# Optimization experiments

Hardware: AMD Instinct MI355X
Metric: run time of the kernel (lower is better)

The kernel has to match this reference:

```python
import jax, jax.numpy as jnp
import numpy as np

N_CAT = 100000
N_USERS = 50000
N_REL = 32
D = 64
E = 1600000
NNZ = 1000000


def setup_inputs() -> dict:
    key = jax.random.key(0)
    ks = jax.random.split(key, 8)
    category_emb = jax.random.normal(ks[0], (N_CAT, D), dtype=jnp.float32)
    user_emb = jax.random.normal(ks[1], (N_USERS, D), dtype=jnp.float32)
    edge_index = jax.random.randint(ks[2], (2, E), 0, N_CAT, dtype=jnp.int64)
    edge_type = jax.random.randint(ks[3], (E,), 1, N_REL + 1, dtype=jnp.int64)  # 1-indexed relations
    im_rows = jax.random.randint(ks[4], (NNZ,), 0, N_USERS, dtype=jnp.int64)
    im_cols = jax.random.randint(ks[5], (NNZ,), 0, N_CAT, dtype=jnp.int64)
    im_vals = jax.random.uniform(ks[6], (NNZ,), dtype=jnp.float32)
    weight = jax.random.normal(ks[7], (N_REL, D), dtype=jnp.float32)
    return {"category_emb": category_emb, "user_emb": user_emb,
            "edge_index": edge_index, "edge_type": edge_type,
            "im_rows": im_rows, "im_cols": im_cols, "im_vals": im_vals,
            "weight": weight}


def reference(category_emb, user_emb, edge_index, edge_type, im_rows, im_cols, im_vals, weight):
    n_categories = category_emb.shape[0]
    n_users = user_emb.shape[0]
    head, tail = edge_index[0], edge_index[1]

    edge_relation_emb = weight[edge_type - 1]                      # [E, D]
    neigh_relation_emb = category_emb[tail] * edge_relation_emb    # [E, D]

    # attention weight: (||h*r|| * ||t*r||)^2 per edge -> scalar per edge
    hr = jnp.linalg.norm(category_emb[head] * edge_relation_emb, axis=1)  # [E]
    tr = jnp.linalg.norm(neigh_relation_emb, axis=1)                      # [E]
    att = (hr * tr) ** 2                                                  # [E]

    # scatter_softmax over edges grouped by head node
    grp_max = jax.ops.segment_max(att, head, num_segments=n_categories)   # [N_CAT]
    e = jnp.exp(att - grp_max[head])                                      # [E]
    grp_sum = jax.ops.segment_sum(e, head, num_segments=n_categories)     # [N_CAT]
    w = e / grp_sum[head]                                                 # [E]

    # scatter_sum aggregation to heads
    category_agg = jax.ops.segment_sum(w[:, None] * neigh_relation_emb,
                                       head, num_segments=n_categories)   # [N_CAT, D]

    # sparse interact_mat @ category_emb (COO)
    user_agg = jax.ops.segment_sum(im_vals[:, None] * category_emb[im_cols],
                                   im_rows, num_segments=n_users)         # [N_USERS, D]

    score = jax.nn.softmax(user_emb @ weight.T, axis=-1)                   # [N_USERS, N_REL]
    user_agg = user_agg + (score @ weight) * user_agg
    return (category_agg, user_agg)
```

## Files before the change

### kernel.cpp

```cpp
#include <hip/hip_runtime.h>
#include <hip/hip_bf16.h>
#include <hip/hip_fp16.h>
#include <float.h>
#include <stdint.h>

#define N_CAT   100000
#define N_USERS 50000
#define N_REL   32
#define D       64
#define NEDGE   1600000
#define NNZ     1000000

#define EB_SHIFT 9
#define EB_SIZE  512
#define NBKE     ((N_CAT + EB_SIZE - 1) / EB_SIZE)
#define UB_SHIFT 8
#define UB_SIZE  256
#define NBKU     ((N_USERS + UB_SIZE - 1) / UB_SIZE)
#define NBK      (NBKE + NBKU)

#define T1   4096
#define ECAP 15360
#define UCAP 7680

#define WSTRIDE 17


__device__ __forceinline__ unsigned int pack_half2(float a, float b) {
    return (unsigned int)__half_as_ushort(__float2half_rn(a)) |
           ((unsigned int)__half_as_ushort(__float2half_rn(b)) << 16);
}

template<int F16>
__device__ __forceinline__ void load_row8(const float4* __restrict__ catv4,
                                          const uint4* __restrict__ cath4,
                                          int row, int gl, float f[8]) {
    if (F16) {
        uint4 h = cath4[(size_t)row * 8 + gl];
        const __half2* hp = (const __half2*)&h;
        float2 a = __half22float2(hp[0]);
        float2 b = __half22float2(hp[1]);
        float2 c = __half22float2(hp[2]);
        float2 d = __half22float2(hp[3]);
        f[0] = a.x; f[1] = a.y; f[2] = b.x; f[3] = b.y;
        f[4] = c.x; f[5] = c.y; f[6] = d.x; f[7] = d.y;
    } else {
        float4 a = catv4[(size_t)row * 16 + gl * 2];
        float4 b = catv4[(size_t)row * 16 + gl * 2 + 1];
        f[0] = a.x; f[1] = a.y; f[2] = a.z; f[3] = a.w;
        f[4] = b.x; f[5] = b.y; f[6] = b.z; f[7] = b.w;
    }
}

__device__ __forceinline__ float reduce_scatter8(const float a[8], int lane) {
    int b3 = (lane >> 3) & 1, b4 = (lane >> 4) & 1, b5 = (lane >> 5) & 1;
    float r[4];
#pragma unroll
    for (int j = 0; j < 4; ++j) {
        float x = b3 ? a[j] : a[j + 4];
        float k = b3 ? a[j + 4] : a[j];
        r[j] = k + __shfl_xor(x, 8);
    }
    float s[2];
#pragma unroll
    for (int j = 0; j < 2; ++j) {
        float x = b4 ? r[j] : r[j + 2];
        float k = b4 ? r[j + 2] : r[j];
        s[j] = k + __shfl_xor(x, 16);
    }
    float x = b5 ? s[0] : s[1];
    float k = b5 ? s[1] : s[0];
    return k + __shfl_xor(x, 32);
}

__device__ __forceinline__ int dim_of_lane(int lane) {
    int g = lane >> 3;
    return ((lane & 7) << 3) | ((g & 1) << 2) | (g & 2) | (g >> 2);
}

template<int W16>
__global__ __launch_bounds__(256) void norm2_kernel(
        const float* __restrict__ cat,
        const float* __restrict__ W,
        float* __restrict__ norm2,
        unsigned short* __restrict__ cath) {
    __shared__ float4 w2[N_REL * 16];
    int t = threadIdx.x;
    const float4* Wv = (const float4*)W;
    for (int i = t; i < N_REL * 16; i += 256) {
        float4 v = Wv[i];
        v.x *= v.x; v.y *= v.y; v.z *= v.z; v.w *= v.w;
        w2[i] = v;
    }
    __syncthreads();

    int node = blockIdx.x * 64 + (t >> 2);
    int q    = t & 3;
    if (node >= N_CAT) return;

    const float4* catv = (const float4*)cat;
    float acc[N_REL];
#pragma unroll
    for (int r = 0; r < N_REL; ++r) acc[r] = 0.f;

    uint2 hp[4];
#pragma unroll
    for (int c = 0; c < 4; ++c) {
        float4 xv = catv[(size_t)node * 16 + q * 4 + c];
        if (W16) {
            hp[c].x = pack_half2(xv.x, xv.y);
            hp[c].y = pack_half2(xv.z, xv.w);
        }
        xv.x *= xv.x; xv.y *= xv.y; xv.z *= xv.z; xv.w *= xv.w;
#pragma unroll
        for (int r = 0; r < N_REL; ++r) {
            float4 wv = w2[r * 16 + q * 4 + c];
            acc[r] += xv.x * wv.x + xv.y * wv.y + xv.z * wv.z + xv.w * wv.w;
        }
    }
    if (W16) {
        uint4* cv16 = (uint4*)cath;
        cv16[(size_t)node * 8 + q * 2]     = make_uint4(hp[0].x, hp[0].y, hp[1].x, hp[1].y);
        cv16[(size_t)node * 8 + q * 2 + 1] = make_uint4(hp[2].x, hp[2].y, hp[3].x, hp[3].y);
    }
#pragma unroll
    for (int r = 0; r < N_REL; ++r) {
        acc[r] += __shfl_xor(acc[r], 1);
        acc[r] += __shfl_xor(acc[r], 2);
    }
    float4* nv = (float4*)norm2;
    size_t base = (size_t)node * 8 + q * 2;
    if (q == 0) {
        nv[base]     = make_float4(acc[0],  acc[1],  acc[2],  acc[3]);
        nv[base + 1] = make_float4(acc[4],  acc[5],  acc[6],  acc[7]);
    } else if (q == 1) {
        nv[base]     = make_float4(acc[8],  acc[9],  acc[10], acc[11]);
        nv[base + 1] = make_float4(acc[12], acc[13], acc[14], acc[15]);
    } else if (q == 2) {
        nv[base]     = make_float4(acc[16], acc[17], acc[18], acc[19]);
        nv[base + 1] = make_float4(acc[20], acc[21], acc[22], acc[23]);
    } else {
        nv[base]     = make_float4(acc[24], acc[25], acc[26], acc[27]);
        nv[base + 1] = make_float4(acc[28], acc[29], acc[30], acc[31]);
    }
}

__global__ void coarse_hist_kernel(const int* __restrict__ head,
                                   const int* __restrict__ imr,
                                   int* __restrict__ ccnt) {
    __shared__ int h[NBK];
    int t = threadIdx.x;
    for (int i = t; i < NBK; i += 256) h[i] = 0;
    __syncthreads();
    int stride = gridDim.x * 256;
    for (int i = blockIdx.x * 256 + t; i < NEDGE + NNZ; i += stride) {
        if (i < NEDGE) atomicAdd(&h[head[i] >> EB_SHIFT], 1);
        else           atomicAdd(&h[NBKE + (imr[i - NEDGE] >> UB_SHIFT)], 1);
    }
    __syncthreads();
    for (int i = t; i < NBK; i += 256) if (h[i]) atomicAdd(&ccnt[i], h[i]);
}

__global__ void coarse_scan_kernel(const int* __restrict__ ccnt,
                                   int* __restrict__ cbase_e, int* __restrict__ cbase_u,
                                   int* __restrict__ ccur_e,  int* __restrict__ ccur_u,
                                   int* __restrict__ offs_e,  int* __restrict__ offs_u) {
    __shared__ int sc[256];
    int t = threadIdx.x;
    int c = (t < NBKE) ? ccnt[t] : 0;
    sc[t] = c; __syncthreads();
    for (int off = 1; off < 256; off <<= 1) {
        int v = (t >= off) ? sc[t - off] : 0; __syncthreads();
        sc[t] += v; __syncthreads();
    }
    int excl = sc[t] - c;
    if (t < NBKE) { cbase_e[t] = excl; ccur_e[t] = excl; }
    if (t == NBKE - 1) cbase_e[NBKE] = excl + c;
    __syncthreads();
    c = (t < NBKU) ? ccnt[NBKE + t] : 0;
    sc[t] = c; __syncthreads();
    for (int off = 1; off < 256; off <<= 1) {
        int v = (t >= off) ? sc[t - off] : 0; __syncthreads();
        sc[t] += v; __syncthreads();
    }
    excl = sc[t] - c;
    if (t < NBKU) { cbase_u[t] = excl; ccur_u[t] = excl; }
    if (t == NBKU - 1) cbase_u[NBKU] = excl + c;
    if (t == 0) { offs_e[N_CAT] = NEDGE; offs_u[N_USERS] = NNZ; }
}

__global__ __launch_bounds__(256) void pass1_edges_kernel(
        const int* __restrict__ head, const int* __restrict__ tail,
        const int* __restrict__ etype, int* __restrict__ ccur_e,
        int* __restrict__ sorted_ta) {
    __shared__ int cnt[256], loc[256], base[256], sc[256];
    __shared__ int stage[T1];
    __shared__ int gpos[T1];
    int t = threadIdx.x;
    int tile = blockIdx.x * T1;
    cnt[t] = 0;
    __syncthreads();
    int rec[16], bk[16];
#pragma unroll
    for (int k = 0; k < 16; ++k) {
        int i = tile + k * 256 + t;
        if (i < NEDGE) {
            int h = head[i], tl = tail[i], r = etype[i] - 1;
            bk[k]  = h >> EB_SHIFT;
            rec[k] = ((h & (EB_SIZE - 1)) << 22) | (tl << 5) | r;
            atomicAdd(&cnt[bk[k]], 1);
        } else bk[k] = -1;
    }
    __syncthreads();
    int c = cnt[t];
    sc[t] = c; __syncthreads();
    for (int off = 1; off < 256; off <<= 1) {
        int v = (t >= off) ? sc[t - off] : 0; __syncthreads();
        sc[t] += v; __syncthreads();
    }
    loc[t] = sc[t] - c;
    if (t < NBKE && c > 0) base[t] = atomicAdd(&ccur_e[t], c);
    __syncthreads();
    cnt[t] = loc[t];
    __syncthreads();
#pragma unroll
    for (int k = 0; k < 16; ++k) {
        if (bk[k] >= 0) {
            int p = atomicAdd(&cnt[bk[k]], 1);
            stage[p] = rec[k];
            gpos[p]  = base[bk[k]] + (p - loc[bk[k]]);
        }
    }
    __syncthreads();
    int nv = min(T1, NEDGE - tile);
    for (int i = t; i < nv; i += 256) sorted_ta[gpos[i]] = stage[i];
}

__global__ __launch_bounds__(256) void pass1_users_kernel(
        const int* __restrict__ imr, const int* __restrict__ imc,
        const float* __restrict__ imv, int* __restrict__ ccur_u,
        int2* __restrict__ sorted_cv) {
    __shared__ int cnt[256], loc[256], base[256], sc[256];
    __shared__ int2 stage[T1];
    __shared__ int gpos[T1];
    int t = threadIdx.x;
    int tile = blockIdx.x * T1;
    cnt[t] = 0;
    __syncthreads();
    int2 rec[16]; int bk[16];
#pragma unroll
    for (int k = 0; k < 16; ++k) {
        int i = tile + k * 256 + t;
        if (i < NNZ) {
            int rr = imr[i];
            bk[k]  = rr >> UB_SHIFT;
            rec[k] = make_int2(((rr & (UB_SIZE - 1)) << 17) | imc[i],
                               __float_as_int(imv[i]));
            atomicAdd(&cnt[bk[k]], 1);
        } else bk[k] = -1;
    }
    __syncthreads();
    int c = cnt[t];
    sc[t] = c; __syncthreads();
    for (int off = 1; off < 256; off <<= 1) {
        int v = (t >= off) ? sc[t - off] : 0; __syncthreads();
        sc[t] += v; __syncthreads();
    }
    loc[t] = sc[t] - c;
    if (t < NBKU && c > 0) base[t] = atomicAdd(&ccur_u[t], c);
    __syncthreads();
    cnt[t] = loc[t];
    __syncthreads();
#pragma unroll
    for (int k = 0; k < 16; ++k) {
        if (bk[k] >= 0) {
            int p = atomicAdd(&cnt[bk[k]], 1);
            stage[p] = rec[k];
            gpos[p]  = base[bk[k]] + (p - loc[bk[k]]);
        }
    }
    __syncthreads();
    int nv = min(T1, NNZ - tile);
    for (int i = t; i < nv; i += 256) sorted_cv[gpos[i]] = stage[i];
}

__global__ __launch_bounds__(256) void pass2_kernel(
        const int* __restrict__ cbase_e, const int* __restrict__ cbase_u,
        int* __restrict__ offs_e, int* __restrict__ offs_u,
        int* __restrict__ sorted_ta, int2* __restrict__ sorted_cv) {
    __shared__ int lds[UCAP * 2];
    __shared__ int fh[EB_SIZE + 1];
    __shared__ int sc[256];
    int t = threadIdx.x;
    int b = blockIdx.x;
    if (b < NBKE) {
        int h0 = b << EB_SHIFT;
        int start = cbase_e[b], end = cbase_e[b + 1];
        int n = min(end - start, ECAP);
        for (int i = t; i < n; i += 256) lds[i] = sorted_ta[start + i];
        fh[2 * t] = 0; fh[2 * t + 1] = 0;
        __syncthreads();
        for (int i = t; i < n; i += 256) atomicAdd(&fh[lds[i] >> 22], 1);
        __syncthreads();
        int a = fh[2 * t], b2 = fh[2 * t + 1];
        sc[t] = a + b2; __syncthreads();
        for (int off = 1; off < 256; off <<= 1) {
            int v = (t >= off) ? sc[t - off] : 0; __syncthreads();
            sc[t] += v; __syncthreads();
        }
        int pe = sc[t] - (a + b2);
        int lim = min(EB_SIZE, N_CAT - h0);
        if (2 * t     < lim) offs_e[h0 + 2 * t]     = start + pe;
        if (2 * t + 1 < lim) offs_e[h0 + 2 * t + 1] = start + pe + a;
        fh[2 * t] = pe; fh[2 * t + 1] = pe + a;
        __syncthreads();
        for (int i = t; i < n; i += 256) {
            int rec = lds[i];
            int p = atomicAdd(&fh[rec >> 22], 1);
            sorted_ta[start + p] = rec & 0x3FFFFF;
        }
    } else {
        int k = b - NBKE;
        int u0 = k << UB_SHIFT;
        int start = cbase_u[k], end = cbase_u[k + 1];
        int n = min(end - start, UCAP);
        int2* lds2 = (int2*)lds;
        for (int i = t; i < n; i += 256) lds2[i] = sorted_cv[start + i];
        fh[t] = 0;
        __syncthreads();
        for (int i = t; i < n; i += 256) atomicAdd(&fh[lds2[i].x >> 17], 1);
        __syncthreads();
        int c = fh[t];
        sc[t] = c; __syncthreads();
        for (int off = 1; off < 256; off <<= 1) {
            int v = (t >= off) ? sc[t - off] : 0; __syncthreads();
            sc[t] += v; __syncthreads();
        }
        int excl = sc[t] - c;
        int lim = min(UB_SIZE, N_USERS - u0);
        if (t < lim) offs_u[u0 + t] = start + excl;
        fh[t] = excl;
        __syncthreads();
        for (int i = t; i < n; i += 256) {
            int2 rec = lds2[i];
            int p = atomicAdd(&fh[rec.x >> 17], 1);
            sorted_cv[start + p] = make_int2(rec.x & 0x1FFFF, rec.y);
        }
    }
}

#define FMA8(ACC, WS, F, W0, W1)                                         \
    ACC[0] += WS * F[0] * W0.x;  ACC[1] += WS * F[1] * W0.y;             \
    ACC[2] += WS * F[2] * W0.z;  ACC[3] += WS * F[3] * W0.w;             \
    ACC[4] += WS * F[4] * W1.x;  ACC[5] += WS * F[5] * W1.y;             \
    ACC[6] += WS * F[6] * W1.z;  ACC[7] += WS * F[7] * W1.w;

__global__ __launch_bounds__(256) void scale_kernel(
        const float* __restrict__ uemb,
        const float* __restrict__ W,
        float* __restrict__ uagg) {
    __shared__ float4 sW[N_REL * 16];
    int t = threadIdx.x;
    const float4* Wv = (const float4*)W;
    for (int i = t; i < N_REL * 16; i += 256) sW[i] = Wv[i];
    __syncthreads();

    int u = blockIdx.x * 64 + (t >> 2);
    int q = t & 3;
    if (u >= N_USERS) return;

    const float4* ur4 = (const float4*)(uemb + (size_t)u * D);
    float acc[N_REL];
#pragma unroll
    for (int r = 0; r < N_REL; ++r) acc[r] = 0.f;

#pragma unroll 1
    for (int c = 0; c < 4; ++c) {
        float4 uv = ur4[q * 4 + c];
#pragma unroll 4
        for (int r = 0; r < N_REL; ++r) {
            float4 w4 = sW[r * 16 + q * 4 + c];
            acc[r] += uv.x * w4.x + uv.y * w4.y + uv.z * w4.z + uv.w * w4.w;
        }
    }
#pragma unroll
    for (int r = 0; r < N_REL; ++r) {
        acc[r] += __shfl_xor(acc[r], 1);
        acc[r] += __shfl_xor(acc[r], 2);
    }
    float m = acc[0];
#pragma unroll
    for (int r = 1; r < N_REL; ++r) m = fmaxf(m, acc[r]);
    float s = 0.f;
#pragma unroll
    for (int r = 0; r < N_REL; ++r) { acc[r] = __expf(acc[r] - m); s += acc[r]; }
    float inv = 1.f / s;

    float4* out4 = (float4*)(uagg + (size_t)u * D);
#pragma unroll 1
    for (int c = 0; c < 4; ++c) {
        float px = 0.f, py = 0.f, pz = 0.f, pw = 0.f;
#pragma unroll 4
        for (int r = 0; r < N_REL; ++r) {
            float4 w4 = sW[r * 16 + c * 4 + q];
            px += acc[r] * w4.x; py += acc[r] * w4.y;
            pz += acc[r] * w4.z; pw += acc[r] * w4.w;
        }
        out4[c * 4 + q] = make_float4(1.f + px * inv, 1.f + py * inv,
                                      1.f + pz * inv, 1.f + pw * inv);
    }
}

template<int F16>
__global__ __launch_bounds__(256, 4) void cat_agg_sorted_kernel(
        const int* __restrict__ offs_e,
        const int* __restrict__ sorted_ta,
        const float* __restrict__ norm2,
        const float* __restrict__ cat,
        const uint4* __restrict__ cath4,
        const float* __restrict__ W,
        float* __restrict__ cat_agg) {
    __shared__ float4 sW4[N_REL * WSTRIDE];
    __shared__ float  scr[4][D];
    {
        const float4* Wv = (const float4*)W;
        for (int i = threadIdx.x; i < N_REL * 16; i += 256)
            sW4[(i >> 4) * WSTRIDE + (i & 15)] = Wv[i];
    }
    __syncthreads();

    const float4* catv4 = (const float4*)cat;
    int wv   = threadIdx.x >> 6;
    int lane = threadIdx.x & 63;
    int grp  = lane >> 3;
    int gl   = lane & 7;
    int h = blockIdx.x * 4 + wv;
    int start = offs_e[h];
    int end   = offs_e[h + 1];
    int deg   = end - start;

    float accA[8], accB[8];
#pragma unroll
    for (int k = 0; k < 8; ++k) { accA[k] = 0.f; accB[k] = 0.f; }

    if (deg <= 32) {
        int rec = 0;
        if (lane < deg) rec = sorted_ta[start + lane];
        int tt = rec >> 5, r = rec & 31;
        float n2t = norm2[(size_t)tt * N_REL + r];
        float n2h = norm2[(size_t)h  * N_REL + r];

        int tA0 = __shfl(rec, grp),      tB0 = __shfl(rec, 8 + grp);
        float fA0[8], fB0[8], fA1[8], fB1[8];
        load_row8<F16>(catv4, cath4, tA0 >> 5, gl, fA0);
        load_row8<F16>(catv4, cath4, tB0 >> 5, gl, fB0);
        int tA1 = 0, tB1 = 0;
        if (deg > 16) {
            tA1 = __shfl(rec, 16 + grp); tB1 = __shfl(rec, 24 + grp);
            load_row8<F16>(catv4, cath4, tA1 >> 5, gl, fA1);
            load_row8<F16>(catv4, cath4, tB1 >> 5, gl, fB1);
        }

        float att = (lane < deg) ? n2h * n2t : -FLT_MAX;
        float m = att;
        m = fmaxf(m, __shfl_xor(m, 1));
        m = fmaxf(m, __shfl_xor(m, 2));
        m = fmaxf(m, __shfl_xor(m, 4));
        m = fmaxf(m, __shfl_xor(m, 8));
        if (deg > 16) m = fmaxf(m, __shfl_xor(m, 16));
        float ex = (lane < deg) ? __expf(att - m) : 0.f;
        float ssum = ex;
        ssum += __shfl_xor(ssum, 1);
        ssum += __shfl_xor(ssum, 2);
        ssum += __shfl_xor(ssum, 4);
        ssum += __shfl_xor(ssum, 8);
        if (deg > 16) ssum += __shfl_xor(ssum, 16);
        float w = (deg > 0) ? ex / ssum : 0.f;

        float wA0 = __shfl(w, grp), wB0 = __shfl(w, 8 + grp);
        const float4* wrA0 = &sW4[(tA0 & 31) * WSTRIDE + gl * 2];
        const float4* wrB0 = &sW4[(tB0 & 31) * WSTRIDE + gl * 2];
        float4 wa00 = wrA0[0], wa01 = wrA0[1];
        float4 wb00 = wrB0[0], wb01 = wrB0[1];
        FMA8(accA, wA0, fA0, wa00, wa01)
        FMA8(accB, wB0, fB0, wb00, wb01)
        if (deg > 16) {
            float wA1 = __shfl(w, 16 + grp), wB1 = __shfl(w, 24 + grp);
            const float4* wrA1 = &sW4[(tA1 & 31) * WSTRIDE + gl * 2];
            const float4* wrB1 = &sW4[(tB1 & 31) * WSTRIDE + gl * 2];
            float4 wa10 = wrA1[0], wa11 = wrA1[1];
            float4 wb10 = wrB1[0], wb11 = wrB1[1];
            FMA8(accA, wA1, fA1, wa10, wa11)
            FMA8(accB, wB1, fB1, wb10, wb11)
        }
    } else if (deg <= 64) {
        int   rec = 0;
        float att = -FLT_MAX;
        if (lane < deg) {
            rec = sorted_ta[start + lane];
            int tt = rec >> 5, r = rec & 31;
            att = norm2[h * N_REL + r] * norm2[(size_t)tt * N_REL + r];
        }
        float m = att;
#pragma unroll
        for (int off = 32; off > 0; off >>= 1) m = fmaxf(m, __shfl_xor(m, off));
        float ex = (lane < deg) ? __expf(att - m) : 0.f;
        float ssum = ex;
#pragma unroll
        for (int off = 32; off > 0; off >>= 1) ssum += __shfl_xor(ssum, off);
        float w = (deg > 0) ? ex / ssum : 0.f;

        for (int e = 0; e < deg; e += 16) {
            int   tA = __shfl(rec, e + grp);
            float wA = __shfl(w,   e + grp);
            int   tB = __shfl(rec, e + 8 + grp);
            float wB = __shfl(w,   e + 8 + grp);
            float fA[8], fB[8];
            load_row8<F16>(catv4, cath4, tA >> 5, gl, fA);
            load_row8<F16>(catv4, cath4, tB >> 5, gl, fB);
            const float4* wrA = &sW4[(tA & 31) * WSTRIDE + gl * 2];
            const float4* wrB = &sW4[(tB & 31) * WSTRIDE + gl * 2];
            float4 wa0 = wrA[0], wa1 = wrA[1];
            float4 wb0 = wrB[0], wb1 = wrB[1];
            FMA8(accA, wA, fA, wa0, wa1)
            FMA8(accB, wB, fB, wb0, wb1)
        }
    } else {
        float m = -FLT_MAX;
        for (int j = lane; j < deg; j += 64) {
            int rec = sorted_ta[start + j];
            int tt = rec >> 5, r = rec & 31;
            m = fmaxf(m, norm2[h * N_REL + r] * norm2[(size_t)tt * N_REL + r]);
        }
#pragma unroll
        for (int off = 32; off > 0; off >>= 1) m = fmaxf(m, __shfl_xor(m, off));
        float ssum = 0.f;
        for (int j = lane; j < deg; j += 64) {
            int rec = sorted_ta[start + j];
            int tt = rec >> 5, r = rec & 31;
            ssum += __expf(norm2[h * N_REL + r] * norm2[(size_t)tt * N_REL + r] - m);
        }
#pragma unroll
        for (int off = 32; off > 0; off >>= 1) ssum += __shfl_xor(ssum, off);
        float inv = 1.f / ssum;
        for (int j0 = 0; j0 < deg; j0 += 64) {
            int n = min(64, deg - j0);
            int   rec = 0;
            float w   = 0.f;
            if (lane < n) {
                rec = sorted_ta[start + j0 + lane];
                int tt = rec >> 5, r = rec & 31;
                w = __expf(norm2[h * N_REL + r] * norm2[(size_t)tt * N_REL + r] - m) * inv;
            }
            for (int e = 0; e < n; e += 16) {
                int   tA = __shfl(rec, e + grp);
                float wA = __shfl(w,   e + grp);
                int   tB = __shfl(rec, e + 8 + grp);
                float wB = __shfl(w,   e + 8 + grp);
                float fA[8], fB[8];
                load_row8<F16>(catv4, cath4, tA >> 5, gl, fA);
                load_row8<F16>(catv4, cath4, tB >> 5, gl, fB);
                const float4* wrA = &sW4[(tA & 31) * WSTRIDE + gl * 2];
                const float4* wrB = &sW4[(tB & 31) * WSTRIDE + gl * 2];
                float4 wa0 = wrA[0], wa1 = wrA[1];
                float4 wb0 = wrB[0], wb1 = wrB[1];
                FMA8(accA, wA, fA, wa0, wa1)
                FMA8(accB, wB, fB, wb0, wb1)
            }
        }
    }

    float a[8];
#pragma unroll
    for (int k = 0; k < 8; ++k) a[k] = accA[k] + accB[k];
    float tot = reduce_scatter8(a, lane);
    scr[wv][dim_of_lane(lane)] = tot;
    if (lane < 16) {
        float4 o = ((const float4*)scr[wv])[lane];
        ((float4*)&cat_agg[(size_t)h * D])[lane] = o;
    }
}

template<int F16>
__global__ __launch_bounds__(256, 4) void spmm_user_kernel(
        const int* __restrict__ offs_u,
        const int2* __restrict__ sorted_cv,
        const float* __restrict__ cat,
        const uint4* __restrict__ cath4,
        float* __restrict__ uagg) {
    __shared__ float scr[4][D];
    const float4* catv4 = (const float4*)cat;
    int wv   = threadIdx.x >> 6;
    int lane = threadIdx.x & 63;
    int grp  = lane >> 3;
    int gl   = lane & 7;
    int u = blockIdx.x * 4 + wv;
    int start = offs_u[u];
    int end   = offs_u[u + 1];
    int deg   = end - start;

    float accA[8], accB[8];
#pragma unroll
    for (int k = 0; k < 8; ++k) { accA[k] = 0.f; accB[k] = 0.f; }

    if (deg <= 32) {
        int my_c = 0; float my_v = 0.f;
        if (lane < deg) {
            int2 cv = sorted_cv[start + lane];
            my_c = cv.x;
            my_v = __int_as_float(cv.y);
        }
        int   cA0 = __shfl(my_c, grp),     cB0 = __shfl(my_c, 8 + grp);
        float vA0 = __shfl(my_v, grp),     vB0 = __shfl(my_v, 8 + grp);
        float fA0[8], fB0[8], fA1[8], fB1[8];
        load_row8<F16>(catv4, cath4, cA0, gl, fA0);
        load_row8<F16>(catv4, cath4, cB0, gl, fB0);
        float vA1 = 0.f, vB1 = 0.f;
        if (deg > 16) {
            int cA1 = __shfl(my_c, 16 + grp), cB1 = __shfl(my_c, 24 + grp);
            vA1 = __shfl(my_v, 16 + grp); vB1 = __shfl(my_v, 24 + grp);
            load_row8<F16>(catv4, cath4, cA1, gl, fA1);
            load_row8<F16>(catv4, cath4, cB1, gl, fB1);
#pragma unroll
            for (int k = 0; k < 8; ++k) {
                accA[k] += vA1 * fA1[k];
                accB[k] += vB1 * fB1[k];
            }
        }
#pragma unroll
        for (int k = 0; k < 8; ++k) {
            accA[k] += vA0 * fA0[k];
            accB[k] += vB0 * fB0[k];
        }
    } else {
        for (int j0 = 0; j0 < deg; j0 += 64) {
            int n = min(64, deg - j0);
            int   my_c = 0;
            float my_v = 0.f;
            if (lane < n) {
                int2 cv = sorted_cv[start + j0 + lane];
                my_c = cv.x;
                my_v = __int_as_float(cv.y);
            }
            for (int e = 0; e < n; e += 16) {
                int   cA = __shfl(my_c, e + grp);
                float vA = __shfl(my_v, e + grp);
                int   cB = __shfl(my_c, e + 8 + grp);
                float vB = __shfl(my_v, e + 8 + grp);
                float fA[8], fB[8];
                load_row8<F16>(catv4, cath4, cA, gl, fA);
                load_row8<F16>(catv4, cath4, cB, gl, fB);
#pragma unroll
                for (int k = 0; k < 8; ++k) {
                    accA[k] += vA * fA[k];
                    accB[k] += vB * fB[k];
                }
            }
        }
    }

    float a[8];
#pragma unroll
    for (int k = 0; k < 8; ++k) a[k] = accA[k] + accB[k];
    float tot = reduce_scatter8(a, lane);
    scr[wv][dim_of_lane(lane)] = tot;
    if (lane < 16) {
        float4 o = ((const float4*)scr[wv])[lane];
        float4* row = (float4*)&uagg[(size_t)u * D];
        float4 s = row[lane];
        row[lane] = make_float4(o.x * s.x, o.y * s.y, o.z * s.z, o.w * s.w);
    }
}

extern "C" void kernel_launch(void* const* d_in, const int* in_sizes, int n_in,
                              void* d_out, int out_size, void* d_ws, size_t ws_size,
                              hipStream_t stream) {
    const float* cat   = (const float*)d_in[0];
    const float* uemb  = (const float*)d_in[1];
    const int*   eidx  = (const int*)d_in[2];
    const int*   etype = (const int*)d_in[3];
    const int*   imr   = (const int*)d_in[4];
    const int*   imc   = (const int*)d_in[5];
    const float* imv   = (const float*)d_in[6];
    const float* W     = (const float*)d_in[7];
    const int* head = eidx;
    const int* tail = eidx + NEDGE;

    float* out     = (float*)d_out;
    float* cat_agg = out;
    float* uagg    = out + (size_t)N_CAT * D;

    float* norm2   = (float*)d_ws;
    int*   ccnt    = (int*)(norm2 + (size_t)N_CAT * N_REL);
    int*   cbase_e = ccnt + NBK;
    int*   cbase_u = cbase_e + NBKE + 1;
    int*   ccur_e  = cbase_u + NBKU + 1;
    int*   ccur_u  = ccur_e + NBKE;
    int*   offs_e  = ccur_u + NBKU;
    int*   offs_u  = offs_e + N_CAT + 1;
    int*   sorted_ta = offs_u + N_USERS + 1;
    int2*  sorted_cv = (int2*)(sorted_ta + NEDGE);

    unsigned short* cath_us =
        (unsigned short*)(((uintptr_t)(sorted_cv + NNZ) + 255) & ~(uintptr_t)255);
    size_t need = (size_t)((char*)(cath_us + (size_t)N_CAT * D) - (char*)d_ws);
    int use16 = (ws_size >= need);

    hipMemsetAsync(ccnt, 0, (size_t)NBK * sizeof(int), stream);

    coarse_hist_kernel<<<512, 256, 0, stream>>>(head, imr, ccnt);
    coarse_scan_kernel<<<1, 256, 0, stream>>>(ccnt, cbase_e, cbase_u,
                                              ccur_e, ccur_u, offs_e, offs_u);
    pass1_edges_kernel<<<(NEDGE + T1 - 1) / T1, 256, 0, stream>>>(
        head, tail, etype, ccur_e, sorted_ta);
    pass1_users_kernel<<<(NNZ + T1 - 1) / T1, 256, 0, stream>>>(
        imr, imc, imv, ccur_u, sorted_cv);
    pass2_kernel<<<NBK, 256, 0, stream>>>(cbase_e, cbase_u, offs_e, offs_u,
                                          sorted_ta, sorted_cv);
    scale_kernel<<<(N_USERS + 63) / 64, 256, 0, stream>>>(uemb, W, uagg);
    if (use16) {
        norm2_kernel<1><<<(N_CAT + 63) / 64, 256, 0, stream>>>(cat, W, norm2, cath_us);
        cat_agg_sorted_kernel<1><<<N_CAT / 4, 256, 0, stream>>>(
            offs_e, sorted_ta, norm2, cat, (const uint4*)cath_us, W, cat_agg);
        spmm_user_kernel<1><<<N_USERS / 4, 256, 0, stream>>>(
            offs_u, sorted_cv, cat, (const uint4*)cath_us, uagg);
    } else {
        norm2_kernel<0><<<(N_CAT + 63) / 64, 256, 0, stream>>>(cat, W, norm2, nullptr);
        cat_agg_sorted_kernel<0><<<N_CAT / 4, 256, 0, stream>>>(
            offs_e, sorted_ta, norm2, cat, nullptr, W, cat_agg);
        spmm_user_kernel<0><<<N_USERS / 4, 256, 0, stream>>>(
            offs_u, sorted_cv, cat, nullptr, uagg);
    }
}
```

Baseline: 310.2 us.

## Replace two-level bucket sort with global-atomic counting sort for CSR build

Replaces the coarse-bucket histogram, LDS-staged pass1 scatter and per-bucket pass2 refinement with a fine-grained global-atomic histogram, a two-block scan of per-node counts, and a direct atomic scatter into final CSR positions. This cuts kernel launches and the second read/write pass over the sorted arrays. In exchange it issues heavily contended global atomics, runs a serial-chunk scan in only two blocks, and makes uncoalesced random writes. Edge order within a segment also becomes nondeterministic, which can change float summation order.

```diff
diff --git a/kernel.cpp b/kernel.cpp
--- a/kernel.cpp
+++ b/kernel.cpp
@@ -10,18 +10,6 @@
 #define D       64
 #define NEDGE   1600000
 #define NNZ     1000000
-
-#define EB_SHIFT 9
-#define EB_SIZE  512
-#define NBKE     ((N_CAT + EB_SIZE - 1) / EB_SIZE)
-#define UB_SHIFT 8
-#define UB_SIZE  256
-#define NBKU     ((N_USERS + UB_SIZE - 1) / UB_SIZE)
-#define NBK      (NBKE + NBKU)
-
-#define T1   4096
-#define ECAP 15360
-#define UCAP 7680
 
 #define WSTRIDE 17
 
@@ -145,206 +133,64 @@
     }
 }
 
-__global__ void coarse_hist_kernel(const int* __restrict__ head,
-                                   const int* __restrict__ imr,
-                                   int* __restrict__ ccnt) {
-    __shared__ int h[NBK];
+__global__ __launch_bounds__(256) void hist_kernel(
+        const int* __restrict__ head, const int* __restrict__ imr,
+        int* __restrict__ cnt_e, int* __restrict__ cnt_u) {
+    int stride = gridDim.x * 256;
+    for (int i = blockIdx.x * 256 + threadIdx.x; i < NEDGE + NNZ; i += stride) {
+        if (i < NEDGE) atomicAdd(&cnt_e[head[i]], 1);
+        else           atomicAdd(&cnt_u[imr[i - NEDGE]], 1);
+    }
+}
+
+__device__ __forceinline__ void scan_one(const int* __restrict__ cnt, int n,
+                                         int* __restrict__ offs,
+                                         int* __restrict__ cur) {
+    __shared__ int part[1024];
     int t = threadIdx.x;
-    for (int i = t; i < NBK; i += 256) h[i] = 0;
-    __syncthreads();
+    int chunk = (n + 1023) / 1024;
+    int lo = t * chunk, hi = min(lo + chunk, n);
+    int s = 0;
+    for (int i = lo; i < hi; ++i) s += cnt[i];
+    part[t] = s; __syncthreads();
+    for (int off = 1; off < 1024; off <<= 1) {
+        int v = (t >= off) ? part[t - off] : 0; __syncthreads();
+        part[t] += v; __syncthreads();
+    }
+    int base = part[t] - s;
+    for (int i = lo; i < hi; ++i) {
+        offs[i] = base; cur[i] = base;
+        base += cnt[i];
+    }
+    if (t == 1023) offs[n] = part[1023];
+}
+
+__global__ __launch_bounds__(1024) void scan2_kernel(
+        const int* __restrict__ cnt_e, const int* __restrict__ cnt_u,
+        int* __restrict__ offs_e, int* __restrict__ offs_u,
+        int* __restrict__ cur_e,  int* __restrict__ cur_u) {
+    if (blockIdx.x == 0) scan_one(cnt_e, N_CAT,   offs_e, cur_e);
+    else                 scan_one(cnt_u, N_USERS, offs_u, cur_u);
+}
+
+__global__ __launch_bounds__(256) void scatter_kernel(
+        const int* __restrict__ head, const int* __restrict__ tail,
+        const int* __restrict__ etype,
+        const int* __restrict__ imr, const int* __restrict__ imc,
+        const float* __restrict__ imv,
+        int* __restrict__ cur_e, int* __restrict__ cur_u,
+        int* __restrict__ sorted_ta, int2* __restrict__ sorted_cv) {
     int stride = gridDim.x * 256;
-    for (int i = blockIdx.x * 256 + t; i < NEDGE + NNZ; i += stride) {
-        if (i < NEDGE) atomicAdd(&h[head[i] >> EB_SHIFT], 1);
-        else           atomicAdd(&h[NBKE + (imr[i - NEDGE] >> UB_SHIFT)], 1);
-    }
-    __syncthreads();
-    for (int i = t; i < NBK; i += 256) if (h[i]) atomicAdd(&ccnt[i], h[i]);
-}
-
-__global__ void coarse_scan_kernel(const int* __restrict__ ccnt,
-                                   int* __restrict__ cbase_e, int* __restrict__ cbase_u,
-                                   int* __restrict__ ccur_e,  int* __restrict__ ccur_u,
-                                   int* __restrict__ offs_e,  int* __restrict__ offs_u) {
-    __shared__ int sc[256];
-    int t = threadIdx.x;
-    int c = (t < NBKE) ? ccnt[t] : 0;
-    sc[t] = c; __syncthreads();
-    for (int off = 1; off < 256; off <<= 1) {
-        int v = (t >= off) ? sc[t - off] : 0; __syncthreads();
-        sc[t] += v; __syncthreads();
-    }
-    int excl = sc[t] - c;
-    if (t < NBKE) { cbase_e[t] = excl; ccur_e[t] = excl; }
-    if (t == NBKE - 1) cbase_e[NBKE] = excl + c;
-    __syncthreads();
-    c = (t < NBKU) ? ccnt[NBKE + t] : 0;
-    sc[t] = c; __syncthreads();
-    for (int off = 1; off < 256; off <<= 1) {
-        int v = (t >= off) ? sc[t - off] : 0; __syncthreads();
-        sc[t] += v; __syncthreads();
-    }
-    excl = sc[t] - c;
-    if (t < NBKU) { cbase_u[t] = excl; ccur_u[t] = excl; }
-    if (t == NBKU - 1) cbase_u[NBKU] = excl + c;
-    if (t == 0) { offs_e[N_CAT] = NEDGE; offs_u[N_USERS] = NNZ; }
-}
-
-__global__ __launch_bounds__(256) void pass1_edges_kernel(
-        const int* __restrict__ head, const int* __restrict__ tail,
-        const int* __restrict__ etype, int* __restrict__ ccur_e,
-        int* __restrict__ sorted_ta) {
-    __shared__ int cnt[256], loc[256], base[256], sc[256];
-    __shared__ int stage[T1];
-    __shared__ int gpos[T1];
-    int t = threadIdx.x;
-    int tile = blockIdx.x * T1;
-    cnt[t] = 0;
-    __syncthreads();
-    int rec[16], bk[16];
-#pragma unroll
-    for (int k = 0; k < 16; ++k) {
-        int i = tile + k * 256 + t;
+    for (int i = blockIdx.x * 256 + threadIdx.x; i < NEDGE + NNZ; i += stride) {
         if (i < NEDGE) {
-            int h = head[i], tl = tail[i], r = etype[i] - 1;
-            bk[k]  = h >> EB_SHIFT;
-            rec[k] = ((h & (EB_SIZE - 1)) << 22) | (tl << 5) | r;
-            atomicAdd(&cnt[bk[k]], 1);
-        } else bk[k] = -1;
-    }
-    __syncthreads();
-    int c = cnt[t];
-    sc[t] = c; __syncthreads();
-    for (int off = 1; off < 256; off <<= 1) {
-        int v = (t >= off) ? sc[t - off] : 0; __syncthreads();
-        sc[t] += v; __syncthreads();
-    }
-    loc[t] = sc[t] - c;
-    if (t < NBKE && c > 0) base[t] = atomicAdd(&ccur_e[t], c);
-    __syncthreads();
-    cnt[t] = loc[t];
-    __syncthreads();
-#pragma unroll
-    for (int k = 0; k < 16; ++k) {
-        if (bk[k] >= 0) {
-            int p = atomicAdd(&cnt[bk[k]], 1);
-            stage[p] = rec[k];
-            gpos[p]  = base[bk[k]] + (p - loc[bk[k]]);
-        }
-    }
-    __syncthreads();
-    int nv = min(T1, NEDGE - tile);
-    for (int i = t; i < nv; i += 256) sorted_ta[gpos[i]] = stage[i];
-}
-
-__global__ __launch_bounds__(256) void pass1_users_kernel(
-        const int* __restrict__ imr, const int* __restrict__ imc,
-        const float* __restrict__ imv, int* __restrict__ ccur_u,
-        int2* __restrict__ sorted_cv) {
-    __shared__ int cnt[256], loc[256], base[256], sc[256];
-    __shared__ int2 stage[T1];
-    __shared__ int gpos[T1];
-    int t = threadIdx.x;
-    int tile = blockIdx.x * T1;
-    cnt[t] = 0;
-    __syncthreads();
-    int2 rec[16]; int bk[16];
-#pragma unroll
-    for (int k = 0; k < 16; ++k) {
-        int i = tile + k * 256 + t;
-        if (i < NNZ) {
-            int rr = imr[i];
-            bk[k]  = rr >> UB_SHIFT;
-            rec[k] = make_int2(((rr & (UB_SIZE - 1)) << 17) | imc[i],
-                               __float_as_int(imv[i]));
-            atomicAdd(&cnt[bk[k]], 1);
-        } else bk[k] = -1;
-    }
-    __syncthreads();
-    int c = cnt[t];
-    sc[t] = c; __syncthreads();
-    for (int off = 1; off < 256; off <<= 1) {
-        int v = (t >= off) ? sc[t - off] : 0; __syncthreads();
-        sc[t] += v; __syncthreads();
-    }
-    loc[t] = sc[t] - c;
-    if (t < NBKU && c > 0) base[t] = atomicAdd(&ccur_u[t], c);
-    __syncthreads();
-    cnt[t] = loc[t];
-    __syncthreads();
-#pragma unroll
-    for (int k = 0; k < 16; ++k) {
-        if (bk[k] >= 0) {
-            int p = atomicAdd(&cnt[bk[k]], 1);
-            stage[p] = rec[k];
-            gpos[p]  = base[bk[k]] + (p - loc[bk[k]]);
-        }
-    }
-    __syncthreads();
-    int nv = min(T1, NNZ - tile);
-    for (int i = t; i < nv; i += 256) sorted_cv[gpos[i]] = stage[i];
-}
-
-__global__ __launch_bounds__(256) void pass2_kernel(
-        const int* __restrict__ cbase_e, const int* __restrict__ cbase_u,
-        int* __restrict__ offs_e, int* __restrict__ offs_u,
-        int* __restrict__ sorted_ta, int2* __restrict__ sorted_cv) {
-    __shared__ int lds[UCAP * 2];
-    __shared__ int fh[EB_SIZE + 1];
-    __shared__ int sc[256];
-    int t = threadIdx.x;
-    int b = blockIdx.x;
-    if (b < NBKE) {
-        int h0 = b << EB_SHIFT;
-        int start = cbase_e[b], end = cbase_e[b + 1];
-        int n = min(end - start, ECAP);
-        for (int i = t; i < n; i += 256) lds[i] = sorted_ta[start + i];
-        fh[2 * t] = 0; fh[2 * t + 1] = 0;
-        __syncthreads();
-        for (int i = t; i < n; i += 256) atomicAdd(&fh[lds[i] >> 22], 1);
-        __syncthreads();
-        int a = fh[2 * t], b2 = fh[2 * t + 1];
-        sc[t] = a + b2; __syncthreads();
-        for (int off = 1; off < 256; off <<= 1) {
-            int v = (t >= off) ? sc[t - off] : 0; __syncthreads();
-            sc[t] += v; __syncthreads();
-        }
-        int pe = sc[t] - (a + b2);
-        int lim = min(EB_SIZE, N_CAT - h0);
-        if (2 * t     < lim) offs_e[h0 + 2 * t]     = start + pe;
-        if (2 * t + 1 < lim) offs_e[h0 + 2 * t + 1] = start + pe + a;
-        fh[2 * t] = pe; fh[2 * t + 1] = pe + a;
-        __syncthreads();
-        for (int i = t; i < n; i += 256) {
-            int rec = lds[i];
-            int p = atomicAdd(&fh[rec >> 22], 1);
-            sorted_ta[start + p] = rec & 0x3FFFFF;
-        }
-    } else {
-        int k = b - NBKE;
-        int u0 = k << UB_SHIFT;
-        int start = cbase_u[k], end = cbase_u[k + 1];
-        int n = min(end - start, UCAP);
-        int2* lds2 = (int2*)lds;
-        for (int i = t; i < n; i += 256) lds2[i] = sorted_cv[start + i];
-        fh[t] = 0;
-        __syncthreads();
-        for (int i = t; i < n; i += 256) atomicAdd(&fh[lds2[i].x >> 17], 1);
-        __syncthreads();
-        int c = fh[t];
-        sc[t] = c; __syncthreads();
-        for (int off = 1; off < 256; off <<= 1) {
-            int v = (t >= off) ? sc[t - off] : 0; __syncthreads();
-            sc[t] += v; __syncthreads();
-        }
-        int excl = sc[t] - c;
-        int lim = min(UB_SIZE, N_USERS - u0);
-        if (t < lim) offs_u[u0 + t] = start + excl;
-        fh[t] = excl;
-        __syncthreads();
-        for (int i = t; i < n; i += 256) {
-            int2 rec = lds2[i];
-            int p = atomicAdd(&fh[rec.x >> 17], 1);
-            sorted_cv[start + p] = make_int2(rec.x & 0x1FFFF, rec.y);
+            int h = head[i];
+            int p = atomicAdd(&cur_e[h], 1);
+            sorted_ta[p] = (tail[i] << 5) | (etype[i] - 1);
+        } else {
+            int j = i - NEDGE;
+            int rr = imr[j];
+            int p = atomicAdd(&cur_u[rr], 1);
+            sorted_cv[p] = make_int2(imc[j], __float_as_int(imv[j]));
         }
     }
 }
@@ -691,12 +537,11 @@
     float* uagg    = out + (size_t)N_CAT * D;
 
     float* norm2   = (float*)d_ws;
-    int*   ccnt    = (int*)(norm2 + (size_t)N_CAT * N_REL);
-    int*   cbase_e = ccnt + NBK;
-    int*   cbase_u = cbase_e + NBKE + 1;
-    int*   ccur_e  = cbase_u + NBKU + 1;
-    int*   ccur_u  = ccur_e + NBKE;
-    int*   offs_e  = ccur_u + NBKU;
+    int*   cnt_e   = (int*)(norm2 + (size_t)N_CAT * N_REL);
+    int*   cnt_u   = cnt_e + N_CAT;
+    int*   cur_e   = cnt_u + N_USERS;
+    int*   cur_u   = cur_e + N_CAT;
+    int*   offs_e  = cur_u + N_USERS;
     int*   offs_u  = offs_e + N_CAT + 1;
     int*   sorted_ta = offs_u + N_USERS + 1;
     int2*  sorted_cv = (int2*)(sorted_ta + NEDGE);
@@ -706,17 +551,12 @@
     size_t need = (size_t)((char*)(cath_us + (size_t)N_CAT * D) - (char*)d_ws);
     int use16 = (ws_size >= need);
 
-    hipMemsetAsync(ccnt, 0, (size_t)NBK * sizeof(int), stream);
-
-    coarse_hist_kernel<<<512, 256, 0, stream>>>(head, imr, ccnt);
-    coarse_scan_kernel<<<1, 256, 0, stream>>>(ccnt, cbase_e, cbase_u,
-                                              ccur_e, ccur_u, offs_e, offs_u);
-    pass1_edges_kernel<<<(NEDGE + T1 - 1) / T1, 256, 0, stream>>>(
-        head, tail, etype, ccur_e, sorted_ta);
-    pass1_users_kernel<<<(NNZ + T1 - 1) / T1, 256, 0, stream>>>(
-        imr, imc, imv, ccur_u, sorted_cv);
-    pass2_kernel<<<NBK, 256, 0, stream>>>(cbase_e, cbase_u, offs_e, offs_u,
-                                          sorted_ta, sorted_cv);
+    hipMemsetAsync(cnt_e, 0, (size_t)(N_CAT + N_USERS) * sizeof(int), stream);
+
+    hist_kernel<<<2048, 256, 0, stream>>>(head, imr, cnt_e, cnt_u);
+    scan2_kernel<<<2, 1024, 0, stream>>>(cnt_e, cnt_u, offs_e, offs_u, cur_e, cur_u);
+    scatter_kernel<<<2048, 256, 0, stream>>>(head, tail, etype, imr, imc, imv,
+                                             cur_e, cur_u, sorted_ta, sorted_cv);
     scale_kernel<<<(N_USERS + 63) / 64, 256, 0, stream>>>(uemb, W, uagg);
     if (use16) {
         norm2_kernel<1><<<(N_CAT + 63) / 64, 256, 0, stream>>>(cat, W, norm2, cath_us);
```

Result: slower. 766.8 us (+147.2%).
